# Optimization experiments

Measured on AMD Instinct MI355X. Metric: run time of the kernel, lower is better.

## Reference

```python
import jax, jax.numpy as jnp
import numpy as np

B, S, D, H, DFF = 2, 2048, 1024, 16, 4096
DH = D // H
EPS = 1e-8


def _alibi_bias(num_heads, seq_len, dtype=jnp.float32):
    # ALiBi slopes for power-of-two head counts: 2^(-8*(h+1)/H)
    h = jnp.arange(1, num_heads + 1, dtype=dtype)
    slopes = jnp.exp2(-8.0 * h / num_heads)          # [H]
    pos = jnp.arange(seq_len, dtype=dtype)
    rel = jnp.abs(pos[None, :] - pos[:, None])       # [S, S] |i-j|
    return -slopes[:, None, None] * rel[None]        # [H, S, S]


def _rmsnorm(x, scale):
    rms = jax.lax.rsqrt(jnp.mean(x * x, axis=-1, keepdims=True) + EPS)
    return scale * x * rms


def setup_inputs() -> dict:
    key = jax.random.key(0)
    ks = jax.random.split(key, 12)
    sd = 0.02
    return {
        "x": jax.random.normal(ks[0], (B, S, D), jnp.float32),
        "scale1": jnp.ones((D,), jnp.float32),
        "scale2": jnp.ones((D,), jnp.float32),
        "w_qkv": jax.random.normal(ks[1], (D, 3 * D), jnp.float32) * sd,
        "b_qkv": jnp.zeros((3 * D,), jnp.float32),
        "w_out": jax.random.normal(ks[2], (D, D), jnp.float32) * sd,
        "b_out": jnp.zeros((D,), jnp.float32),
        "w1": jax.random.normal(ks[3], (D, DFF), jnp.float32) * sd,
        "b1": jnp.zeros((DFF,), jnp.float32),
        "w2": jax.random.normal(ks[4], (DFF, D), jnp.float32) * sd,
        "b2": jnp.zeros((D,), jnp.float32),
    }


def reference(x, scale1, scale2, w_qkv, b_qkv, w_out, b_out, w1, b1, w2, b2):
    residual = x
    xn = _rmsnorm(x, scale1)
    qkv = xn @ w_qkv + b_qkv                                  # [B,S,3D]
    q, k, v = jnp.split(qkv, 3, axis=-1)
    def heads(t):
        return t.reshape(B, S, H, DH).transpose(0, 2, 1, 3)   # [B,H,S,DH]
    q, k, v = heads(q), heads(k), heads(v)
    scores = jnp.einsum("bhsd,bhtd->bhst", q, k) / (DH ** 0.5)
    scores = scores + _alibi_bias(H, S, scores.dtype)[None]
    attn = jax.nn.softmax(scores, axis=-1)
    out = jnp.einsum("bhst,bhtd->bhsd", attn, v)              # [B,H,S,DH]
    out = out.transpose(0, 2, 1, 3).reshape(B, S, D)
    x = residual + (out @ w_out + b_out)
    residual = x
    xn = _rmsnorm(x, scale2)
    h = jax.nn.gelu(xn @ w1 + b1, approximate=False)
    return residual + (h @ w2 + b2)
```

## Files before the change

### kernel.cpp

```cpp
#include <hip/hip_runtime.h>
#include <hip/hip_bf16.h>
#include <math.h>

#define B_ 2
#define S_ 2048
#define D_ 1024
#define H_ 16
#define DH_ 64
#define DFF_ 4096
#define M_ (B_*S_)

typedef __bf16 bf16;
typedef __bf16 bf16x8 __attribute__((ext_vector_type(8)));
typedef __bf16 bf16x4 __attribute__((ext_vector_type(4)));
typedef float f32x4 __attribute__((ext_vector_type(4)));

__device__ __forceinline__ void gll16(const void* g, void* l) {
  __builtin_amdgcn_global_load_lds(
      (const __attribute__((address_space(1))) void*)g,
      (__attribute__((address_space(3))) void*)l, 16, 0, 0);
}

#define WAITCNT_VM4 0xF74
#define WAITCNT_VM0 0xF70

__global__ __launch_bounds__(256) void rmsnorm_kernel(const float* __restrict__ x,
    const float* __restrict__ scale, bf16* __restrict__ out) {
  __shared__ float red[4];
  int row = blockIdx.x, t = threadIdx.x;
  const float4* xr = (const float4*)(x + (size_t)row * D_);
  float4 v = xr[t];
  float ss = v.x*v.x + v.y*v.y + v.z*v.z + v.w*v.w;
  #pragma unroll
  for (int off = 32; off > 0; off >>= 1) ss += __shfl_down(ss, off, 64);
  if ((t & 63) == 0) red[t >> 6] = ss;
  __syncthreads();
  float tot = red[0] + red[1] + red[2] + red[3];
  float r = rsqrtf(tot * (1.0f / D_) + 1e-8f);
  float4 sc = ((const float4*)scale)[t];
  bf16x4 o;
  o[0] = (bf16)(v.x * sc.x * r);
  o[1] = (bf16)(v.y * sc.y * r);
  o[2] = (bf16)(v.z * sc.z * r);
  o[3] = (bf16)(v.w * sc.w * r);
  *(bf16x4*)(out + (size_t)row * D_ + t * 4) = o;
}

__global__ __launch_bounds__(256) void reduce_rms_kernel(
    const bf16* __restrict__ p0, const bf16* __restrict__ p1,
    const float* __restrict__ x, const float* __restrict__ bias,
    const float* __restrict__ scale, float* __restrict__ x2, bf16* __restrict__ xn2) {
  __shared__ float red[4];
  int row = blockIdx.x, t = threadIdx.x;
  float4 xv = ((const float4*)(x + (size_t)row * D_))[t];
  float4 bv = ((const float4*)bias)[t];
  bf16x4 a = *(const bf16x4*)(p0 + (size_t)row * D_ + t * 4);
  bf16x4 b = *(const bf16x4*)(p1 + (size_t)row * D_ + t * 4);
  float s0 = xv.x + bv.x + (float)a[0] + (float)b[0];
  float s1 = xv.y + bv.y + (float)a[1] + (float)b[1];
  float s2 = xv.z + bv.z + (float)a[2] + (float)b[2];
  float s3 = xv.w + bv.w + (float)a[3] + (float)b[3];
  float4 o; o.x = s0; o.y = s1; o.z = s2; o.w = s3;
  ((float4*)(x2 + (size_t)row * D_))[t] = o;
  float ss = s0*s0 + s1*s1 + s2*s2 + s3*s3;
  #pragma unroll
  for (int off = 32; off > 0; off >>= 1) ss += __shfl_down(ss, off, 64);
  if ((t & 63) == 0) red[t >> 6] = ss;
  __syncthreads();
  float tot = red[0] + red[1] + red[2] + red[3];
  float r = rsqrtf(tot * (1.0f / D_) + 1e-8f);
  float4 sc = ((const float4*)scale)[t];
  bf16x4 on;
  on[0] = (bf16)(s0 * sc.x * r);
  on[1] = (bf16)(s1 * sc.y * r);
  on[2] = (bf16)(s2 * sc.z * r);
  on[3] = (bf16)(s3 * sc.w * r);
  *(bf16x4*)(xn2 + (size_t)row * D_ + t * 4) = on;
}

__global__ __launch_bounds__(256) void reduce_out_kernel(
    const bf16* __restrict__ p0, const bf16* __restrict__ p1,
    const float* __restrict__ x2, const float* __restrict__ bias,
    float* __restrict__ dout) {
  int row = blockIdx.x, t = threadIdx.x;
  float4 xv = ((const float4*)(x2 + (size_t)row * D_))[t];
  float4 bv = ((const float4*)bias)[t];
  bf16x4 a = *(const bf16x4*)(p0 + (size_t)row * D_ + t * 4);
  bf16x4 b = *(const bf16x4*)(p1 + (size_t)row * D_ + t * 4);
  float4 o;
  o.x = xv.x + bv.x + (float)a[0] + (float)b[0];
  o.y = xv.y + bv.y + (float)a[1] + (float)b[1];
  o.z = xv.z + bv.z + (float)a[2] + (float)b[2];
  o.w = xv.w + bv.w + (float)a[3] + (float)b[3];
  ((float4*)(dout + (size_t)row * D_))[t] = o;
}

__global__ __launch_bounds__(256) void wtrans_kernel(const float* __restrict__ W,
    bf16* __restrict__ Wt, int K, int N) {
  __shared__ float tile[32][33];
  int n0 = blockIdx.x * 32, k0 = blockIdx.y * 32;
  int tx = threadIdx.x & 31, ty = threadIdx.x >> 5;
  #pragma unroll
  for (int i = 0; i < 4; i++)
    tile[ty + i*8][tx] = W[(size_t)(k0 + ty + i*8) * N + n0 + tx];
  __syncthreads();
  #pragma unroll
  for (int i = 0; i < 4; i++)
    Wt[(size_t)(n0 + ty + i*8) * K + k0 + tx] = (bf16)tile[tx][ty + i*8];
}

__global__ __launch_bounds__(256) void vtrans_kernel(const bf16* __restrict__ Vin,
    bf16* __restrict__ Vt) {
  __shared__ bf16 tile[32][34];
  size_t base = (size_t)blockIdx.z * (S_ * DH_);
  int s0 = blockIdx.x * 32, d0 = blockIdx.y * 32;
  int tx = threadIdx.x & 31, ty = threadIdx.x >> 5;
  #pragma unroll
  for (int i = 0; i < 4; i++)
    tile[ty + i*8][tx] = Vin[base + (size_t)(s0 + ty + i*8) * DH_ + d0 + tx];
  __syncthreads();
  #pragma unroll
  for (int i = 0; i < 4; i++)
    Vt[base + (size_t)(d0 + ty + i*8) * S_ + s0 + tx] = tile[tx][ty + i*8];
}

__device__ __forceinline__ float gelu_fast(float x) {
  float e = __builtin_amdgcn_exp2f(2.3022585093f * x * (1.0f + 0.044715f * x * x));
  return x * e / (1.0f + e);
}

template<int MODE>
__global__ __launch_bounds__(256) void gemm_kernel(
    const bf16* __restrict__ A, const bf16* __restrict__ Bt,
    const float* __restrict__ bias, void* __restrict__ outp, void* __restrict__ outp2,
    int M, int N, int K, int lda) {
  __shared__ __align__(16) bf16 As[3][128 * 32];
  __shared__ __align__(16) bf16 Bs[3][128 * 32];
  int t = threadIdx.x;
  int wave = t >> 6, lane = t & 63;
  int lm = lane & 15, lg = lane >> 4;
  int m0 = blockIdx.y * 128, n0 = blockIdx.x * 128;
  size_t koff = (size_t)blockIdx.z * K;
  int wm = (wave >> 1) * 64, wn = (wave & 1) * 64;
  f32x4 acc[4][4] = {};

  int srow = t >> 2, sslot = t & 3;
  int scol = (sslot ^ ((srow >> 1) & 3)) * 8;
  const bf16* Ag = A + (size_t)(m0 + srow) * lda + koff + scol;
  const bf16* Bg = Bt + (size_t)(n0 + srow) * lda + koff + scol;
  size_t half = (size_t)64 * lda;
  int rsw = (lm >> 1) & 3;
  int nk = K >> 5;

  gll16(Ag, As[0] + t * 8);
  gll16(Ag + half, As[0] + 2048 + t * 8);
  gll16(Bg, Bs[0] + t * 8);
  gll16(Bg + half, Bs[0] + 2048 + t * 8);
  if (nk > 1) {
    gll16(Ag + 32, As[1] + t * 8);
    gll16(Ag + 32 + half, As[1] + 2048 + t * 8);
    gll16(Bg + 32, Bs[1] + t * 8);
    gll16(Bg + 32 + half, Bs[1] + 2048 + t * 8);
  }

  int buf = 0;
  for (int j = 0; j < nk; ++j) {
    if (j + 1 < nk) __builtin_amdgcn_s_waitcnt(WAITCNT_VM4);
    else            __builtin_amdgcn_s_waitcnt(WAITCNT_VM0);
    __builtin_amdgcn_s_barrier();
    if (j + 2 < nk) {
      int k2 = (j + 2) << 5;
      int nbuf = buf + 2; if (nbuf >= 3) nbuf -= 3;
      bf16* Ad = As[nbuf];
      bf16* Bd = Bs[nbuf];
      gll16(Ag + k2, Ad + t * 8);
      gll16(Ag + k2 + half, Ad + 2048 + t * 8);
      gll16(Bg + k2, Bd + t * 8);
      gll16(Bg + k2 + half, Bd + 2048 + t * 8);
    }
    const bf16* Ab = As[buf];
    const bf16* Bb = Bs[buf];
    if (++buf == 3) buf = 0;
    bf16x8 af[4], bfr[4];
    #pragma unroll
    for (int i = 0; i < 4; i++)
      af[i] = *(const bf16x8*)(Ab + (wm + i * 16 + lm) * 32 + (lg ^ rsw) * 8);
    #pragma unroll
    for (int j2 = 0; j2 < 4; j2++)
      bfr[j2] = *(const bf16x8*)(Bb + (wn + j2 * 16 + lm) * 32 + (lg ^ rsw) * 8);
    #pragma unroll
    for (int i = 0; i < 4; i++)
      #pragma unroll
      for (int j2 = 0; j2 < 4; j2++)
        acc[i][j2] = __builtin_amdgcn_mfma_f32_16x16x32_bf16(af[i], bfr[j2], acc[i][j2], 0, 0, 0);
  }

  bf16* pout = (MODE == 5) ? ((blockIdx.z == 0) ? (bf16*)outp : (bf16*)outp2) : (bf16*)outp;

  #pragma unroll
  for (int i = 0; i < 4; i++) {
    int row = m0 + wm + i * 16 + lg * 4;
    #pragma unroll
    for (int j = 0; j < 4; j++) {
      int col = n0 + wn + j * 16 + lm;
      float bcol = (MODE == 5) ? 0.f : bias[col];
      #pragma unroll
      for (int r = 0; r < 4; r++) {
        float v = acc[i][j][r] + bcol;
        int rr = row + r;
        if (MODE == 0) {
          int which = col >> 10, d = col & 1023;
          int hh = d >> 6, dh = d & 63;
          int bb = rr >> 11, s = rr & 2047;
          ((bf16*)outp)[(size_t)which * ((size_t)B_*H_*S_*DH_) +
              ((size_t)(bb * H_ + hh) * S_ + s) * DH_ + dh] = (bf16)v;
        } else if (MODE == 2) {
          ((bf16*)outp)[(size_t)rr * N + col] = (bf16)gelu_fast(v);
        } else {
          pout[(size_t)rr * N + col] = (bf16)v;
        }
      }
    }
  }
}

#define PSTR 68
__global__ __launch_bounds__(256, 3) void attn_kernel(
    const bf16* __restrict__ q, const bf16* __restrict__ k,
    const bf16* __restrict__ vT, bf16* __restrict__ pbuf, float* __restrict__ rsbuf) {
  __shared__ __align__(16) bf16 Ks[2][64 * 64];
  __shared__ __align__(16) bf16 Vs[2][64 * 64];
  __shared__ __align__(16) bf16 Ps[4 * 16 * PSTR];
  int t = threadIdx.x, wave = t >> 6, lane = t & 63;
  int lm = lane & 15, lg = lane >> 4;
  int qt = blockIdx.x, q0 = qt * 64;
  int h = 15 - blockIdx.y;
  int b = blockIdx.z >> 1, c = blockIdx.z & 1;
  size_t base = (size_t)(b * H_ + h) * ((size_t)S_ * DH_);
  const bf16* Q = q + base;
  const bf16* K = k + base;
  const bf16* V = vT + base;
  const float LOG2E = 1.4426950408889634f;
  float sl2 = exp2f(-0.5f * (float)(h + 1)) * LOG2E;
  float nslope = -sl2;
  const float qscale = 0.125f * LOG2E;
  const float FMAX = 8.0f;

  int W = (int)(24.0f / sl2);
  int jlo = (q0 - W) >> 6; if (jlo < 0) jlo = 0;
  int jhi = ((q0 + 63 + W) >> 6) + 1; if (jhi > S_ / 64) jhi = S_ / 64;
  int n = jhi - jlo, nc0 = (n + 1) >> 1;
  int cjlo = c ? jlo + nc0 : jlo;
  int cjhi = c ? jhi : jlo + nc0;
  int slot = ((b * H_ + h) * 32 + qt) * 2 + c;
  bf16* Pout = pbuf + (size_t)slot * 4096;
  float* Rout = rsbuf + (size_t)slot * 64;

  if (cjlo >= cjhi) {
    uint4 z = {0, 0, 0, 0};
    *(uint4*)(Pout + t * 8) = z;
    *(uint4*)(Pout + 2048 + t * 8) = z;
    if (t < 64) Rout[t] = 0.f;
    return;
  }

  bf16x8 qf[2];
  #pragma unroll
  for (int h2 = 0; h2 < 2; h2++) {
    bf16x8 v = *(const bf16x8*)(Q + (size_t)(q0 + wave * 16 + lm) * DH_ + h2 * 32 + lg * 8);
    #pragma unroll
    for (int e = 0; e < 8; e++) v[e] = (bf16)((float)v[e] * qscale);
    qf[h2] = v;
  }

  int row0 = t >> 3, jslot = t & 7;
  int gsw = (jslot ^ (row0 & 7)) << 3;
  const bf16* Ksrc0 = K + (size_t)row0 * DH_ + gsw;
  const bf16* Vsrc0 = V + (size_t)row0 * S_ + gsw;

  {
    int jt = cjlo << 6;
    gll16(Ksrc0 + (size_t)jt * DH_, Ks[0] + (size_t)t * 8);
    gll16(Ksrc0 + (size_t)(jt + 32) * DH_, Ks[0] + (size_t)(t + 256) * 8);
    gll16(Vsrc0 + jt, Vs[0] + (size_t)t * 8);
    gll16(Vsrc0 + (size_t)32 * S_ + jt, Vs[0] + (size_t)(t + 256) * 8);
  }

  f32x4 oacc[4] = {};
  float rs[4] = {0.f, 0.f, 0.f, 0.f};
  int psw = lm & 7;

  for (int jj = cjlo; jj < cjhi; ++jj) {
    int buf = (jj - cjlo) & 1;
    int jt = jj << 6;
    __syncthreads();
    if (jj + 1 < cjhi) {
      int jn = (jj + 1) << 6;
      gll16(Ksrc0 + (size_t)jn * DH_, Ks[buf ^ 1] + (size_t)t * 8);
      gll16(Ksrc0 + (size_t)(jn + 32) * DH_, Ks[buf ^ 1] + (size_t)(t + 256) * 8);
      gll16(Vsrc0 + jn, Vs[buf ^ 1] + (size_t)t * 8);
      gll16(Vsrc0 + (size_t)32 * S_ + jn, Vs[buf ^ 1] + (size_t)(t + 256) * 8);
    }
    const bf16* Kb = Ks[buf];
    const bf16* Vb = Vs[buf];

    f32x4 sc[4];
    #pragma unroll
    for (int tt = 0; tt < 4; tt++) {
      f32x4 a = {-FMAX, -FMAX, -FMAX, -FMAX};
      int krow = tt * 16 + lm;
      bf16x8 kb0 = *(const bf16x8*)(Kb + (size_t)(krow * 8 + (lg ^ psw)) * 8);
      bf16x8 kb1 = *(const bf16x8*)(Kb + (size_t)(krow * 8 + ((lg + 4) ^ psw)) * 8);
      a = __builtin_amdgcn_mfma_f32_16x16x32_bf16(qf[0], kb0, a, 0, 0, 0);
      a = __builtin_amdgcn_mfma_f32_16x16x32_bf16(qf[1], kb1, a, 0, 0, 0);
      sc[tt] = a;
    }

    bf16* Pw = Ps + wave * (16 * PSTR);
    int i0 = q0 + wave * 16 + lg * 4;
    #pragma unroll
    for (int tt = 0; tt < 4; tt++) {
      float f0 = (float)(i0 - jt - tt * 16 - lm);
      #pragma unroll
      for (int r = 0; r < 4; r++) {
        float s2 = fmaf(nslope, fabsf(f0 + (float)r), sc[tt][r]);
        float p = __builtin_amdgcn_exp2f(s2);
        rs[r] += p;
        Pw[(lg * 4 + r) * PSTR + tt * 16 + lm] = (bf16)p;
      }
    }

    bf16x8 ap0 = *(const bf16x8*)(Pw + lm * PSTR + lg * 8);
    bf16x8 ap1 = *(const bf16x8*)(Pw + lm * PSTR + 32 + lg * 8);
    #pragma unroll
    for (int tt = 0; tt < 4; tt++) {
      int vrow = tt * 16 + lm;
      bf16x8 vb0 = *(const bf16x8*)(Vb + (size_t)(vrow * 8 + (lg ^ psw)) * 8);
      bf16x8 vb1 = *(const bf16x8*)(Vb + (size_t)(vrow * 8 + ((lg + 4) ^ psw)) * 8);
      oacc[tt] = __builtin_amdgcn_mfma_f32_16x16x32_bf16(ap0, vb0, oacc[tt], 0, 0, 0);
      oacc[tt] = __builtin_amdgcn_mfma_f32_16x16x32_bf16(ap1, vb1, oacc[tt], 0, 0, 0);
    }
  }

  #pragma unroll
  for (int r = 0; r < 4; r++) {
    #pragma unroll
    for (int off = 1; off < 16; off <<= 1)
      rs[r] += __shfl_xor(rs[r], off, 16);
  }

  #pragma unroll
  for (int r = 0; r < 4; r++) {
    int lrow = wave * 16 + lg * 4 + r;
    if (lm == 0) Rout[lrow] = rs[r];
    #pragma unroll
    for (int tt = 0; tt < 4; tt++)
      Pout[lrow * 64 + tt * 16 + lm] = (bf16)oacc[tt][r];
  }
}

__global__ __launch_bounds__(256) void attn_combine_kernel(
    const bf16* __restrict__ pbuf, const float* __restrict__ rsbuf,
    bf16* __restrict__ ao) {
  int qt = blockIdx.x, h = blockIdx.y, b = blockIdx.z;
  int slot0 = ((b * H_ + h) * 32 + qt) * 2;
  int t = threadIdx.x;
  int row = t >> 2, cg = (t & 3) * 16;
  const bf16* P0 = pbuf + (size_t)slot0 * 4096 + row * 64 + cg;
  const bf16* P1 = pbuf + (size_t)(slot0 + 1) * 4096 + row * 64 + cg;
  float inv = 1.0f / (rsbuf[(size_t)slot0 * 64 + row] + rsbuf[(size_t)(slot0 + 1) * 64 + row]);
  bf16x8 a0 = *(const bf16x8*)P0, a1 = *(const bf16x8*)(P0 + 8);
  bf16x8 b0 = *(const bf16x8*)P1, b1 = *(const bf16x8*)(P1 + 8);
  bf16x8 o0, o1;
  #pragma unroll
  for (int e = 0; e < 8; e++) {
    o0[e] = (bf16)(((float)a0[e] + (float)b0[e]) * inv);
    o1[e] = (bf16)(((float)a1[e] + (float)b1[e]) * inv);
  }
  bf16* dst = ao + ((size_t)(b * S_) + qt * 64 + row) * D_ + h * 64 + cg;
  *(bf16x8*)dst = o0;
  *(bf16x8*)(dst + 8) = o1;
}

extern "C" void kernel_launch(void* const* d_in, const int* in_sizes, int n_in,
                              void* d_out, int out_size, void* d_ws, size_t ws_size,
                              hipStream_t stream) {
  const float* x      = (const float*)d_in[0];
  const float* scale1 = (const float*)d_in[1];
  const float* scale2 = (const float*)d_in[2];
  const float* w_qkv  = (const float*)d_in[3];
  const float* b_qkv  = (const float*)d_in[4];
  const float* w_out  = (const float*)d_in[5];
  const float* b_out  = (const float*)d_in[6];
  const float* w1     = (const float*)d_in[7];
  const float* b1     = (const float*)d_in[8];
  const float* w2     = (const float*)d_in[9];
  const float* b2     = (const float*)d_in[10];

  char* ws = (char*)d_ws;
  const size_t MB = 1024 * 1024;
  bf16* xn    = (bf16*)(ws + 0);
  bf16* qb    = (bf16*)(ws + 8*MB);
  bf16* kb    = (bf16*)(ws + 16*MB);
  bf16* vb    = (bf16*)(ws + 24*MB);
  bf16* vT    = (bf16*)(ws + 32*MB);
  bf16* wqkvT = (bf16*)(ws + 40*MB);
  bf16* woutT = (bf16*)(ws + 46*MB);
  bf16* w1T   = (bf16*)(ws + 48*MB);
  bf16* w2T   = (bf16*)(ws + 56*MB);
  float* x2   = (float*)(ws + 64*MB);
  bf16* xn2   = qb;
  bf16* pp0   = kb;
  bf16* pp1   = vb;
  bf16* hbuf  = kb;
  bf16* qp0   = xn;
  bf16* qp1   = w1T;
  bf16* ao    = xn;
  bf16* pbuf  = (bf16*)(ws + 64*MB);
  float* rsbuf = (float*)(ws + 40*MB);

  dim3 blk(256);
  wtrans_kernel<<<dim3(3072/32, 1024/32), blk, 0, stream>>>(w_qkv, wqkvT, 1024, 3072);
  wtrans_kernel<<<dim3(1024/32, 1024/32), blk, 0, stream>>>(w_out, woutT, 1024, 1024);
  wtrans_kernel<<<dim3(4096/32, 1024/32), blk, 0, stream>>>(w1, w1T, 1024, 4096);
  wtrans_kernel<<<dim3(1024/32, 4096/32), blk, 0, stream>>>(w2, w2T, 4096, 1024);

  rmsnorm_kernel<<<dim3(M_), blk, 0, stream>>>(x, scale1, xn);

  gemm_kernel<0><<<dim3(3072/128, M_/128, 1), blk, 0, stream>>>(
      xn, wqkvT, b_qkv, qb, nullptr, M_, 3072, 1024, 1024);

  vtrans_kernel<<<dim3(S_/32, DH_/32, B_*H_), blk, 0, stream>>>(vb, vT);

  attn_kernel<<<dim3(S_/64, H_, B_*2), blk, 0, stream>>>(qb, kb, vT, pbuf, rsbuf);
  attn_combine_kernel<<<dim3(S_/64, H_, B_), blk, 0, stream>>>(pbuf, rsbuf, ao);

  gemm_kernel<5><<<dim3(1024/128, M_/128, 2), blk, 0, stream>>>(
      ao, woutT, nullptr, pp0, pp1, M_, 1024, 512, 1024);
  reduce_rms_kernel<<<dim3(M_), blk, 0, stream>>>(pp0, pp1, x, b_out, scale2, x2, xn2);

  gemm_kernel<2><<<dim3(4096/128, M_/128, 1), blk, 0, stream>>>(
      xn2, w1T, b1, hbuf, nullptr, M_, 4096, 1024, 1024);

  gemm_kernel<5><<<dim3(1024/128, M_/128, 2), blk, 0, stream>>>(
      hbuf, w2T, nullptr, qp0, qp1, M_, 1024, 2048, 4096);
  reduce_out_kernel<<<dim3(M_), blk, 0, stream>>>(qp0, qp1, x2, b2, (float*)d_out);
}
```

Measured before the change: 371.2 us.

## Drop K/V double buffering in attention kernel to raise occupancy

The attention kernel now keeps a single shared-memory buffer for the K and V tiles instead of two. Each tile is loaded synchronously at the start of its iteration, with a barrier before and after the load. Launch bounds go from 3 to 5 blocks per CU to take advantage of the smaller shared-memory footprint. This trades away software prefetch of the next tile for more resident waves to hide load latency, and it adds a barrier per iteration.

```diff
diff --git a/kernel.cpp b/kernel.cpp
--- a/kernel.cpp
+++ b/kernel.cpp
@@ -225,11 +225,11 @@
 }
 
 #define PSTR 68
-__global__ __launch_bounds__(256, 3) void attn_kernel(
+__global__ __launch_bounds__(256, 5) void attn_kernel(
     const bf16* __restrict__ q, const bf16* __restrict__ k,
     const bf16* __restrict__ vT, bf16* __restrict__ pbuf, float* __restrict__ rsbuf) {
-  __shared__ __align__(16) bf16 Ks[2][64 * 64];
-  __shared__ __align__(16) bf16 Vs[2][64 * 64];
+  __shared__ __align__(16) bf16 Ks[64 * 64];
+  __shared__ __align__(16) bf16 Vs[64 * 64];
   __shared__ __align__(16) bf16 Ps[4 * 16 * PSTR];
   int t = threadIdx.x, wave = t >> 6, lane = t & 63;
   int lm = lane & 15, lg = lane >> 4;
@@ -278,39 +278,26 @@
   const bf16* Ksrc0 = K + (size_t)row0 * DH_ + gsw;
   const bf16* Vsrc0 = V + (size_t)row0 * S_ + gsw;
 
-  {
-    int jt = cjlo << 6;
-    gll16(Ksrc0 + (size_t)jt * DH_, Ks[0] + (size_t)t * 8);
-    gll16(Ksrc0 + (size_t)(jt + 32) * DH_, Ks[0] + (size_t)(t + 256) * 8);
-    gll16(Vsrc0 + jt, Vs[0] + (size_t)t * 8);
-    gll16(Vsrc0 + (size_t)32 * S_ + jt, Vs[0] + (size_t)(t + 256) * 8);
-  }
-
   f32x4 oacc[4] = {};
   float rs[4] = {0.f, 0.f, 0.f, 0.f};
   int psw = lm & 7;
 
   for (int jj = cjlo; jj < cjhi; ++jj) {
-    int buf = (jj - cjlo) & 1;
     int jt = jj << 6;
     __syncthreads();
-    if (jj + 1 < cjhi) {
-      int jn = (jj + 1) << 6;
-      gll16(Ksrc0 + (size_t)jn * DH_, Ks[buf ^ 1] + (size_t)t * 8);
-      gll16(Ksrc0 + (size_t)(jn + 32) * DH_, Ks[buf ^ 1] + (size_t)(t + 256) * 8);
-      gll16(Vsrc0 + jn, Vs[buf ^ 1] + (size_t)t * 8);
-      gll16(Vsrc0 + (size_t)32 * S_ + jn, Vs[buf ^ 1] + (size_t)(t + 256) * 8);
-    }
-    const bf16* Kb = Ks[buf];
-    const bf16* Vb = Vs[buf];
+    gll16(Ksrc0 + (size_t)jt * DH_, Ks + (size_t)t * 8);
+    gll16(Ksrc0 + (size_t)(jt + 32) * DH_, Ks + (size_t)(t + 256) * 8);
+    gll16(Vsrc0 + jt, Vs + (size_t)t * 8);
+    gll16(Vsrc0 + (size_t)32 * S_ + jt, Vs + (size_t)(t + 256) * 8);
+    __syncthreads();
 
     f32x4 sc[4];
     #pragma unroll
     for (int tt = 0; tt < 4; tt++) {
       f32x4 a = {-FMAX, -FMAX, -FMAX, -FMAX};
       int krow = tt * 16 + lm;
-      bf16x8 kb0 = *(const bf16x8*)(Kb + (size_t)(krow * 8 + (lg ^ psw)) * 8);
-      bf16x8 kb1 = *(const bf16x8*)(Kb + (size_t)(krow * 8 + ((lg + 4) ^ psw)) * 8);
+      bf16x8 kb0 = *(const bf16x8*)(Ks + (size_t)(krow * 8 + (lg ^ psw)) * 8);
+      bf16x8 kb1 = *(const bf16x8*)(Ks + (size_t)(krow * 8 + ((lg + 4) ^ psw)) * 8);
       a = __builtin_amdgcn_mfma_f32_16x16x32_bf16(qf[0], kb0, a, 0, 0, 0);
       a = __builtin_amdgcn_mfma_f32_16x16x32_bf16(qf[1], kb1, a, 0, 0, 0);
       sc[tt] = a;
@@ -335,8 +322,8 @@
     #pragma unroll
     for (int tt = 0; tt < 4; tt++) {
       int vrow = tt * 16 + lm;
-      bf16x8 vb0 = *(const bf16x8*)(Vb + (size_t)(vrow * 8 + (lg ^ psw)) * 8);
-      bf16x8 vb1 = *(const bf16x8*)(Vb + (size_t)(vrow * 8 + ((lg + 4) ^ psw)) * 8);
+      bf16x8 vb0 = *(const bf16x8*)(Vs + (size_t)(vrow * 8 + (lg ^ psw)) * 8);
+      bf16x8 vb1 = *(const bf16x8*)(Vs + (size_t)(vrow * 8 + ((lg + 4) ^ psw)) * 8);
       oacc[tt] = __builtin_amdgcn_mfma_f32_16x16x32_bf16(ap0, vb0, oacc[tt], 0, 0, 0);
       oacc[tt] = __builtin_amdgcn_mfma_f32_16x16x32_bf16(ap1, vb1, oacc[tt], 0, 0, 0);
     }
```

Result: faster. 361.3 us (-2.7%).
